# Kernel optimization log

Hardware: AMD Instinct MI355X
Metric: run time of the kernel (lower is better)

The kernel has to match this reference:

```python
import jax, jax.numpy as jnp
import numpy as np

B, T, D = 32, 512, 384
DUR_MAX = 8          # durations drawn from [0, DUR_MAX)
MAX_LEN = T * (DUR_MAX - 1)  # 3584, static pad length (= target_mel_len)


def setup_inputs() -> dict:
    key = jax.random.key(0)
    kx, kd = jax.random.split(key)
    x = jax.random.normal(kx, (B, T, D), dtype=jnp.float32)
    duration_target = jax.random.randint(kd, (B, T), 0, DUR_MAX, dtype=jnp.int64)
    return {"x": x, "duration_target": duration_target, "target_mel_len": MAX_LEN}


def reference(x, duration_target, target_mel_len):
    # Effective duration: original does vec.expand(max(int(d), 1), -1),
    # so zero durations still produce one frame.
    eff = jnp.maximum(duration_target, 1)          # [B, T]
    cum = jnp.cumsum(eff, axis=1)                   # [B, T] exclusive upper bounds
    mel_len = cum[:, -1]                            # [B]
    L = int(target_mel_len)                         # static pad length
    frames = jnp.arange(L)                          # [L]
    # frame j belongs to phoneme i where cum[i-1] <= j < cum[i]
    idx = jax.vmap(lambda c: jnp.searchsorted(c, frames, side="right"))(cum)  # [B, L]
    idx = jnp.minimum(idx, x.shape[1] - 1)          # clamp padded region
    out = jnp.take_along_axis(x, idx[:, :, None], axis=1)  # [B, L, D]
    mask = frames[None, :] < mel_len[:, None]       # [B, L]
    out = out * mask[:, :, None].astype(out.dtype)  # zero padding like F.pad
    return out, mel_len.astype(jnp.int64)
```

## Files before the change

### kernel.cpp

```cpp
#include <hip/hip_runtime.h>


#define T_DIM 512
#define D_DIM 384
#define VEC_PER_ROW (D_DIM / 4)

__global__ void __launch_bounds__(T_DIM)
lr_build_map(const int* __restrict__ dur, int* __restrict__ idx_map,
             float* __restrict__ mel_out, int L) {
    const int b = blockIdx.x;
    const int t = threadIdx.x;
    __shared__ int s[T_DIM];

    int d = dur[b * T_DIM + t];
    int e = d > 1 ? d : 1;
    s[t] = e;
    __syncthreads();

    #pragma unroll
    for (int off = 1; off < T_DIM; off <<= 1) {
        int add = (t >= off) ? s[t - off] : 0;
        __syncthreads();
        s[t] += add;
        __syncthreads();
    }

    const int cum   = s[t];
    const int mel   = s[T_DIM - 1];
    const int start = cum - e;

    int* map_b = idx_map + (size_t)b * L;
    for (int k = 0; k < e; ++k)
        map_b[start + k] = t;

    for (int f = mel + t; f < L; f += T_DIM)
        map_b[f] = -1;

    if (t == 0)
        mel_out[b] = (float)mel;
}

__global__ void __launch_bounds__(256)
lr_gather(const float4* __restrict__ x, const int* __restrict__ idx_map,
          float4* __restrict__ out, int L, int vec_per_batch) {
    const int b = blockIdx.y;
    const int g = blockIdx.x * 256 + threadIdx.x;
    if (g >= vec_per_batch) return;

    const int f = g / VEC_PER_ROW;
    const int w = g - f * VEC_PER_ROW;

    const int idx = idx_map[(size_t)b * L + f];
    float4 v = make_float4(0.f, 0.f, 0.f, 0.f);
    if (idx >= 0)
        v = x[((size_t)b * T_DIM + idx) * VEC_PER_ROW + w];
    out[((size_t)b * L + (size_t)f) * VEC_PER_ROW + w] = v;
}

extern "C" void kernel_launch(void* const* d_in, const int* in_sizes, int n_in,
                              void* d_out, int out_size, void* d_ws, size_t ws_size,
                              hipStream_t stream) {
    const float* x   = (const float*)d_in[0];
    const int*   dur = (const int*)d_in[1];

    const int B = in_sizes[1] / T_DIM;
    const int L = (out_size - B) / (B * D_DIM);

    int*   idx_map = (int*)d_ws;
    float* out     = (float*)d_out;
    float* mel_out = out + (size_t)B * L * D_DIM;

    lr_build_map<<<dim3(B), dim3(T_DIM), 0, stream>>>(dur, idx_map, mel_out, L);

    const int vec_per_batch = L * VEC_PER_ROW;
    const int blocks = (vec_per_batch + 255) / 256;
    lr_gather<<<dim3(blocks, B), dim3(256), 0, stream>>>(
        (const float4*)x, idx_map, (float4*)out, L, vec_per_batch);
}
```

Measured before the change: 203.0 us.

## Use wave-shuffle scan, two-vector gather with nontemporal stores and XCD block swizzle

Replaces the shared-memory Hillis-Steele scan in the map builder with a wave-level shuffle scan plus a per-wave sum table, which cuts the number of barriers. The gather kernel now handles two float4 values per thread, writes output with nontemporal stores, and uses a 1D grid whose block index is remapped across 8 groups to spread contiguous work over the XCDs. All shapes are hardcoded as compile-time constants. The aim is to lower store cache pollution and per-thread overhead on a bandwidth-bound ~176MB write, with the risk that the swizzle or the larger per-thread work reduces memory parallelism.

```diff
diff --git a/kernel.cpp b/kernel.cpp
--- a/kernel.cpp
+++ b/kernel.cpp
@@ -1,60 +1,87 @@
 #include <hip/hip_runtime.h>
 
 
+#define B_DIM 32
 #define T_DIM 512
 #define D_DIM 384
-#define VEC_PER_ROW (D_DIM / 4)
+#define L_DIM 3584
+#define VEC_PER_ROW 96
+#define PAIRS_PER_BATCH (L_DIM * VEC_PER_ROW / 2)
+#define GATHER_BLOCK 256
+#define BLOCKS_PER_BATCH (PAIRS_PER_BATCH / GATHER_BLOCK)
+#define GATHER_BLOCKS (BLOCKS_PER_BATCH * B_DIM)
+
+typedef float f32x4 __attribute__((ext_vector_type(4)));
 
 __global__ void __launch_bounds__(T_DIM)
 lr_build_map(const int* __restrict__ dur, int* __restrict__ idx_map,
-             float* __restrict__ mel_out, int L) {
-    const int b = blockIdx.x;
-    const int t = threadIdx.x;
-    __shared__ int s[T_DIM];
+             float* __restrict__ mel_out) {
+    const int b    = blockIdx.x;
+    const int t    = threadIdx.x;
+    const int lane = t & 63;
+    const int wv   = t >> 6;
 
     int d = dur[b * T_DIM + t];
     int e = d > 1 ? d : 1;
-    s[t] = e;
+
+    int val = e;
+    #pragma unroll
+    for (int off = 1; off < 64; off <<= 1) {
+        int n = __shfl_up(val, off, 64);
+        if (lane >= off) val += n;
+    }
+
+    __shared__ int wsum[8];
+    if (lane == 63) wsum[wv] = val;
     __syncthreads();
 
+    int base = 0, tot = 0;
     #pragma unroll
-    for (int off = 1; off < T_DIM; off <<= 1) {
-        int add = (t >= off) ? s[t - off] : 0;
-        __syncthreads();
-        s[t] += add;
-        __syncthreads();
+    for (int i = 0; i < 8; ++i) {
+        int s = wsum[i];
+        tot += s;
+        if (i < wv) base += s;
     }
 
-    const int cum   = s[t];
-    const int mel   = s[T_DIM - 1];
+    const int cum   = val + base;
+    const int mel   = tot;
     const int start = cum - e;
 
-    int* map_b = idx_map + (size_t)b * L;
+    int* map_b = idx_map + b * L_DIM;
     for (int k = 0; k < e; ++k)
         map_b[start + k] = t;
 
-    for (int f = mel + t; f < L; f += T_DIM)
+    for (int f = mel + t; f < L_DIM; f += T_DIM)
         map_b[f] = -1;
 
     if (t == 0)
         mel_out[b] = (float)mel;
 }
 
-__global__ void __launch_bounds__(256)
-lr_gather(const float4* __restrict__ x, const int* __restrict__ idx_map,
-          float4* __restrict__ out, int L, int vec_per_batch) {
-    const int b = blockIdx.y;
-    const int g = blockIdx.x * 256 + threadIdx.x;
-    if (g >= vec_per_batch) return;
+__global__ void __launch_bounds__(GATHER_BLOCK)
+lr_gather(const f32x4* __restrict__ x, const int* __restrict__ idx_map,
+          f32x4* __restrict__ out) {
+    const int bid = blockIdx.x;
+    const int blk = (bid & 7) * (GATHER_BLOCKS / 8) + (bid >> 3);
 
-    const int f = g / VEC_PER_ROW;
-    const int w = g - f * VEC_PER_ROW;
+    const int b    = blk / BLOCKS_PER_BATCH;
+    const int pblk = blk - b * BLOCKS_PER_BATCH;
+    const int p    = pblk * GATHER_BLOCK + threadIdx.x;
+    const int v0   = p << 1;
+    const int f    = v0 / VEC_PER_ROW;
+    const int w    = v0 - f * VEC_PER_ROW;
 
-    const int idx = idx_map[(size_t)b * L + f];
-    float4 v = make_float4(0.f, 0.f, 0.f, 0.f);
-    if (idx >= 0)
-        v = x[((size_t)b * T_DIM + idx) * VEC_PER_ROW + w];
-    out[((size_t)b * L + (size_t)f) * VEC_PER_ROW + w] = v;
+    const int idx = idx_map[b * L_DIM + f];
+    f32x4 a = (f32x4)0.f;
+    f32x4 c = (f32x4)0.f;
+    if (idx >= 0) {
+        const f32x4* row = x + ((b * T_DIM + idx) * VEC_PER_ROW);
+        a = row[w];
+        c = row[w + 1];
+    }
+    f32x4* o = out + (size_t)(b * L_DIM + f) * VEC_PER_ROW + w;
+    __builtin_nontemporal_store(a, o);
+    __builtin_nontemporal_store(c, o + 1);
 }
 
 extern "C" void kernel_launch(void* const* d_in, const int* in_sizes, int n_in,
@@ -63,17 +90,12 @@
     const float* x   = (const float*)d_in[0];
     const int*   dur = (const int*)d_in[1];
 
-    const int B = in_sizes[1] / T_DIM;
-    const int L = (out_size - B) / (B * D_DIM);
-
     int*   idx_map = (int*)d_ws;
     float* out     = (float*)d_out;
-    float* mel_out = out + (size_t)B * L * D_DIM;
+    float* mel_out = out + (size_t)B_DIM * L_DIM * D_DIM;
 
-    lr_build_map<<<dim3(B), dim3(T_DIM), 0, stream>>>(dur, idx_map, mel_out, L);
+    lr_build_map<<<dim3(B_DIM), dim3(T_DIM), 0, stream>>>(dur, idx_map, mel_out);
 
-    const int vec_per_batch = L * VEC_PER_ROW;
-    const int blocks = (vec_per_batch + 255) / 256;
-    lr_gather<<<dim3(blocks, B), dim3(256), 0, stream>>>(
-        (const float4*)x, idx_map, (float4*)out, L, vec_per_batch);
+    lr_gather<<<dim3(GATHER_BLOCKS), dim3(GATHER_BLOCK), 0, stream>>>(
+        (const f32x4*)x, idx_map, (f32x4*)out);
 }
```

New measurement: 221.8 us. 9.3% more time.
